# Performance work log

Hardware: AMD Instinct MI355X
Metric: run time of the kernel (lower is better)

Reference implementation:

```python
import jax, jax.numpy as jnp
import numpy as np

B, T, D, U = 32, 512, 512, 512  # batch, seq_len, input dim, lstm units


def setup_inputs() -> dict:
    key = jax.random.key(0)
    ks = jax.random.split(key, 8)
    s_in = 1.0 / np.sqrt(D)
    s_rec = 1.0 / np.sqrt(U)
    return {
        "x": jax.random.normal(ks[0], (B, T, D), dtype=jnp.float32),
        "z": jax.random.normal(ks[1], (B, U), dtype=jnp.float32) * 0.1,
        # forward-direction LSTM params (Keras gate order: i, f, c, o)
        "Wf": jax.random.normal(ks[2], (D, 4 * U), dtype=jnp.float32) * s_in,
        "Uf": jax.random.normal(ks[3], (U, 4 * U), dtype=jnp.float32) * s_rec,
        "bf": jnp.zeros((4 * U,), dtype=jnp.float32),
        # backward-direction LSTM params
        "Wb": jax.random.normal(ks[4], (D, 4 * U), dtype=jnp.float32) * s_in,
        "Ub": jax.random.normal(ks[5], (U, 4 * U), dtype=jnp.float32) * s_rec,
        "bb": jnp.zeros((4 * U,), dtype=jnp.float32),
    }


def _lstm(x, h0, c0, W, Uw, b, reverse):
    """Single-direction LSTM, return_sequences=True. Keras gate order i,f,c,o."""
    u = h0.shape[-1]
    # precompute input projections for all timesteps in one big GEMM
    xg = jnp.einsum("btd,dk->btk", x, W) + b  # [B,T,4U]

    def step(carry, xg_t):
        h, c = carry
        g = xg_t + h @ Uw  # [B,4U]
        i = jax.nn.sigmoid(g[:, :u])
        f = jax.nn.sigmoid(g[:, u:2 * u])
        cc = jnp.tanh(g[:, 2 * u:3 * u])
        o = jax.nn.sigmoid(g[:, 3 * u:])
        c = f * c + i * cc
        h = o * jnp.tanh(c)
        return (h, c), h

    # scan over time; reverse=True == Keras go_backwards + output re-reversal
    _, hs = jax.lax.scan(step, (h0, c0), jnp.swapaxes(xg, 0, 1), reverse=reverse)
    return jnp.swapaxes(hs, 0, 1)  # [B,T,U]


def reference(x, z, Wf, Uf, bf, Wb, Ub, bb):
    # conditional=True: initial_state = [z, z, z, z] -> both directions get (h0=z, c0=z)
    fwd = _lstm(x, z, z, Wf, Uf, bf, reverse=False)
    bwd = _lstm(x, z, z, Wb, Ub, bb, reverse=True)
    return fwd + bwd  # Bidirectional merge_mode='sum', return_sequences=True
```

## Files before the change

kernel.cpp:

```cpp
#include <hip/hip_runtime.h>
#include <hip/hip_bf16.h>


typedef __attribute__((ext_vector_type(8))) __bf16 bf16x8;
typedef __attribute__((ext_vector_type(4))) __bf16 bf16x4;
typedef __attribute__((ext_vector_type(4))) float fvec4;

#define AS_G(p) ((const __attribute__((address_space(1))) void*)(p))
#define AS_L(p) ((__attribute__((address_space(3))) void*)(p))

__device__ __forceinline__ float sigm(float x) {
  return __builtin_amdgcn_rcpf(1.f + __expf(-x));
}
__device__ __forceinline__ float tanh_f(float x) {
  return 1.f - 2.f * __builtin_amdgcn_rcpf(__expf(2.f * x) + 1.f);
}

__device__ __forceinline__ void st_h4(__bf16* p, float h0, float h1) {
  union { __bf16 h[2]; unsigned int u; } pk;
  pk.h[0] = (__bf16)h0;
  pk.h[1] = (__bf16)h1;
  __hip_atomic_store((unsigned int*)p, pk.u, __ATOMIC_RELAXED, __HIP_MEMORY_SCOPE_AGENT);
}


__global__ void k_convert_x(const float* __restrict__ x, __bf16* __restrict__ xb) {
  size_t i = ((size_t)blockIdx.x * 256 + threadIdx.x) * 8;
  fvec4 a = *(const fvec4*)(x + i);
  fvec4 b = *(const fvec4*)(x + i + 4);
  bf16x8 o;
#pragma unroll
  for (int j = 0; j < 4; ++j) { o[j] = (__bf16)a[j]; o[4 + j] = (__bf16)b[j]; }
  *(bf16x8*)(xb + i) = o;
}

__global__ void k_build_T(const float* __restrict__ src, const float* __restrict__ bvec,
                          __bf16* __restrict__ dst, float* __restrict__ bias_out) {
  int p = blockIdx.x;
  int g = p >> 6, r = p & 63, w = r >> 4, q = r & 15, jj = q >> 2, gate = q & 3;
  int orig = gate * 512 + g * 16 + w * 4 + jj;
  for (int k = threadIdx.x; k < 512; k += 256)
    dst[(size_t)p * 512 + k] = (__bf16)src[(size_t)k * 2048 + orig];
  if (bias_out && threadIdx.x == 0) bias_out[p] = bvec[orig];
}

__global__ void k_init_flags(int* flags) {
  int i = blockIdx.x * 256 + threadIdx.x;
  if (i < 1024) flags[i] = 0;
}

__global__ void k_init_h(const float* __restrict__ z, __bf16* __restrict__ hbuf) {
  int idx = blockIdx.x * 256 + threadIdx.x;
  int dir = idx >> 14, rem = idx & 16383;
  int ks = rem >> 10, row = (rem >> 5) & 31, c = rem & 31;
  hbuf[(size_t)dir * 32768 + rem] = (__bf16)z[row * 512 + ks * 32 + c];
}


__global__ __launch_bounds__(256, 2) void k_gemm_xw(
    const __bf16* __restrict__ A,
    const __bf16* __restrict__ Bt,
    const float* __restrict__ bias,
    __bf16* __restrict__ C)
{
  __shared__ __align__(16) __bf16 As[128 * 32];
  __shared__ __align__(16) __bf16 Bs[128 * 32];
  const int tid = threadIdx.x;
  const int w = tid >> 6, lane = tid & 63, quad = lane >> 4, l15 = lane & 15;
  const int m0 = blockIdx.y * 128, n0 = blockIdx.x * 128;
  const int wm = w & 1, wn = w >> 1;

  fvec4 acc[4][4];
  const fvec4 zero = {0.f, 0.f, 0.f, 0.f};
#pragma unroll
  for (int i = 0; i < 4; ++i)
#pragma unroll
    for (int j = 0; j < 4; ++j) acc[i][j] = zero;

  for (int kb = 0; kb < 16; ++kb) {
    const int k0 = kb * 32;
#pragma unroll
    for (int i = 0; i < 2; ++i) {
      const int c = (i * 4 + w) * 64 + lane;
      const int row = c >> 2, kk = (c & 3) * 8;
      __builtin_amdgcn_global_load_lds(AS_G(A + (size_t)(m0 + row) * 512 + k0 + kk),
                                       AS_L(As + (size_t)(i * 4 + w) * 512), 16, 0, 0);
      __builtin_amdgcn_global_load_lds(AS_G(Bt + (size_t)(n0 + row) * 512 + k0 + kk),
                                       AS_L(Bs + (size_t)(i * 4 + w) * 512), 16, 0, 0);
    }
    __syncthreads();
    bf16x8 af[4], bfr[4];
#pragma unroll
    for (int mt = 0; mt < 4; ++mt)
      af[mt] = *(const bf16x8*)(As + (wm * 64 + mt * 16 + l15) * 32 + quad * 8);
#pragma unroll
    for (int nt = 0; nt < 4; ++nt)
      bfr[nt] = *(const bf16x8*)(Bs + (wn * 64 + nt * 16 + l15) * 32 + quad * 8);
#pragma unroll
    for (int mt = 0; mt < 4; ++mt)
#pragma unroll
      for (int nt = 0; nt < 4; ++nt)
        acc[mt][nt] = __builtin_amdgcn_mfma_f32_16x16x32_bf16(af[mt], bfr[nt], acc[mt][nt], 0, 0, 0);
    __syncthreads();
  }

#pragma unroll
  for (int nt = 0; nt < 4; ++nt) {
    const int col = n0 + wn * 64 + nt * 16 + l15;
    const float bv = bias[col];
#pragma unroll
    for (int mt = 0; mt < 4; ++mt) {
      const int rowb = m0 + wm * 64 + mt * 16 + quad * 4;
#pragma unroll
      for (int r = 0; r < 4; ++r)
        C[(size_t)(rowb + r) * 4096 + col] = (__bf16)(acc[mt][nt][r] + bv);
    }
  }
}


__global__ __launch_bounds__(256, 1) void k_lstm_rec(
    const __bf16* __restrict__ xg,
    const float* __restrict__ z,
    const __bf16* __restrict__ UT,
    __bf16* __restrict__ hbuf,
    float* __restrict__ outf,
    __bf16* __restrict__ outb,
    int* __restrict__ flags)
{
  const int blk = blockIdx.x, dir = blk >> 5, g = blk & 31;
  const int tid = threadIdx.x, w = tid >> 6, lane = tid & 63;
  const int quad = lane >> 4, l15 = lane & 15;
  __shared__ __align__(16) __bf16 h_lds[16384];
  __shared__ __align__(16) float gates[32][68];

  bf16x8 breg[16];
  {
    const __bf16* up = UT + ((size_t)dir * 2048 + g * 64 + w * 16 + l15) * 512 + quad * 8;
#pragma unroll
    for (int ks = 0; ks < 16; ++ks) breg[ks] = *(const bf16x8*)(up + ks * 32);
  }

  const int b = lane >> 1, jpair = lane & 1;
  const int hcol = g * 16 + w * 4 + jpair * 2;
  float c0 = z[b * 512 + hcol];
  float c1 = z[b * 512 + hcol + 1];
  int* myflags = flags + dir * 512;
  const __bf16* hsrc = hbuf + (size_t)dir * 32768;
  const int stoff = (g >> 1) * 1024 + b * 32 + (g & 1) * 16 + w * 4 + jpair * 2;
  const int stage_off = w * 4096 + lane * 8;
  const fvec4 zero = {0.f, 0.f, 0.f, 0.f};

  for (int kt = 0; kt < 512; ++kt) {
    const int t = dir ? (511 - kt) : kt;
    const int pr = kt & 1;

    const bf16x8 xv = *(const bf16x8*)(xg + (size_t)(b * 512 + t) * 4096 +
                                       dir * 2048 + g * 64 + w * 16 + jpair * 8);

    if (kt > 0) {
      const int* fl = myflags + (kt - 1);
      while (__hip_atomic_load(fl, __ATOMIC_RELAXED, __HIP_MEMORY_SCOPE_AGENT) < 32)
        __builtin_amdgcn_s_sleep(1);
    }

    {
      const unsigned long long* src =
          (const unsigned long long*)(hsrc + pr * 16384 + stage_off);
      unsigned long long tmp[16];
#pragma unroll
      for (int it = 0; it < 8; ++it) {
        tmp[2 * it]     = __hip_atomic_load(src + it * 128,
                            __ATOMIC_RELAXED, __HIP_MEMORY_SCOPE_AGENT);
        tmp[2 * it + 1] = __hip_atomic_load(src + it * 128 + 1,
                            __ATOMIC_RELAXED, __HIP_MEMORY_SCOPE_AGENT);
      }
      __bf16* dst = h_lds + stage_off;
#pragma unroll
      for (int it = 0; it < 8; ++it) {
        union { unsigned long long u[2]; bf16x8 v; } cv;
        cv.u[0] = tmp[2 * it];
        cv.u[1] = tmp[2 * it + 1];
        *(bf16x8*)(dst + it * 512) = cv.v;
      }
    }
    __syncthreads();

    fvec4 acc0 = zero, acc1 = zero;
#pragma unroll 8
    for (int ks = 0; ks < 16; ++ks) {
      bf16x8 a0 = *(const bf16x8*)(h_lds + ks * 1024 + l15 * 32 + quad * 8);
      bf16x8 a1 = *(const bf16x8*)(h_lds + ks * 1024 + (16 + l15) * 32 + quad * 8);
      acc0 = __builtin_amdgcn_mfma_f32_16x16x32_bf16(a0, breg[ks], acc0, 0, 0, 0);
      acc1 = __builtin_amdgcn_mfma_f32_16x16x32_bf16(a1, breg[ks], acc1, 0, 0, 0);
    }

#pragma unroll
    for (int r = 0; r < 4; ++r) {
      gates[quad * 4 + r][w * 16 + l15] = acc0[r];
      gates[16 + quad * 4 + r][w * 16 + l15] = acc1[r];
    }
    const fvec4 gA = *(const fvec4*)&gates[b][w * 16 + jpair * 8];
    const fvec4 gB = *(const fvec4*)&gates[b][w * 16 + jpair * 8 + 4];

    float xf[8];
#pragma unroll
    for (int j = 0; j < 8; ++j) xf[j] = (float)xv[j];

    float ii = sigm(gA[0] + xf[0]);
    float ff = sigm(gA[1] + xf[1]);
    float cc = tanh_f(gA[2] + xf[2]);
    float oo = sigm(gA[3] + xf[3]);
    c0 = ff * c0 + ii * cc;
    const float h0 = oo * tanh_f(c0);

    ii = sigm(gB[0] + xf[4]);
    ff = sigm(gB[1] + xf[5]);
    cc = tanh_f(gB[2] + xf[6]);
    oo = sigm(gB[3] + xf[7]);
    c1 = ff * c1 + ii * cc;
    const float h1 = oo * tanh_f(c1);

    st_h4(hbuf + (size_t)dir * 32768 + ((kt + 1) & 1) * 16384 + stoff, h0, h1);

    __syncthreads();
    if (tid == 0)
      __hip_atomic_fetch_add(myflags + kt, 1, __ATOMIC_RELAXED, __HIP_MEMORY_SCOPE_AGENT);

    const size_t oidx = (size_t)(b * 512 + t) * 512 + hcol;
    if (dir == 0) {
      outf[oidx] = h0;
      outf[oidx + 1] = h1;
    } else {
      outb[oidx] = (__bf16)h0;
      outb[oidx + 1] = (__bf16)h1;
    }
  }
}


__global__ void k_add_bwd(float* __restrict__ out, const __bf16* __restrict__ outb) {
  size_t i = ((size_t)blockIdx.x * 256 + threadIdx.x) * 4;
  if (i >= (size_t)32 * 512 * 512) return;
  fvec4 o = *(const fvec4*)(out + i);
  bf16x4 bv = *(const bf16x4*)(outb + i);
#pragma unroll
  for (int j = 0; j < 4; ++j) o[j] += (float)bv[j];
  *(fvec4*)(out + i) = o;
}


extern "C" void kernel_launch(void* const* d_in, const int* in_sizes, int n_in,
                              void* d_out, int out_size, void* d_ws, size_t ws_size,
                              hipStream_t stream) {
  const float* x  = (const float*)d_in[0];
  const float* z  = (const float*)d_in[1];
  const float* Wf = (const float*)d_in[2];
  const float* Uf = (const float*)d_in[3];
  const float* bf = (const float*)d_in[4];
  const float* Wb = (const float*)d_in[5];
  const float* Ub = (const float*)d_in[6];
  const float* bb = (const float*)d_in[7];
  float* out = (float*)d_out;
  char* ws = (char*)d_ws;

  size_t off = 0;
  __bf16* xg    = (__bf16*)(ws + off); off += (size_t)16384 * 4096 * 2;
  __bf16* UT    = (__bf16*)(ws + off); off += (size_t)2 * 2048 * 512 * 2;
  __bf16* hbuf  = (__bf16*)(ws + off); off += (size_t)2 * 2 * 16384 * 2;
  int*    flags = (int*)(ws + off);    off += 4096;
  float*  biasp = (float*)(ws + off);  off += 4096 * 4;
  char* uni = ws + off;
  __bf16* xb   = (__bf16*)uni;
  __bf16* WT   = (__bf16*)(uni + (size_t)16384 * 512 * 2);
  __bf16* outb = (__bf16*)uni;

  k_convert_x<<<4096, 256, 0, stream>>>(x, xb);
  k_build_T<<<2048, 256, 0, stream>>>(Wf, bf, WT, biasp);
  k_build_T<<<2048, 256, 0, stream>>>(Wb, bb, WT + (size_t)2048 * 512, biasp + 2048);
  k_build_T<<<2048, 256, 0, stream>>>(Uf, nullptr, UT, nullptr);
  k_build_T<<<2048, 256, 0, stream>>>(Ub, nullptr, UT + (size_t)2048 * 512, nullptr);
  k_init_flags<<<4, 256, 0, stream>>>(flags);
  k_init_h<<<128, 256, 0, stream>>>(z, hbuf);
  k_gemm_xw<<<dim3(32, 128), 256, 0, stream>>>(xb, WT, biasp, xg);
  k_lstm_rec<<<64, 256, 0, stream>>>(xg, z, UT, hbuf, out, outb, flags);
  k_add_bwd<<<8192, 256, 0, stream>>>(out, outb);
}
```

Before: 2.266 ms.

## Replace atomic step counter with per-block mailbox flags and swizzle LDS h tile

Cross-block step synchronization changes from one shared atomic counter per timestep to a mailbox matrix. Each block stores its completed step into a private slot, and wave 0 polls all producers' slots in parallel with a ballot before a block barrier. This removes contention from 32 blocks atomically incrementing the same word each step. The staged hidden-state tile in LDS is also XOR-swizzled so the MFMA A-fragment reads hit fewer bank conflicts. The trade-off is an extra barrier per step and more polling traffic.

Result: faster. 2.205 ms (-2.7%).

```diff
diff --git a/kernel.cpp b/kernel.cpp
--- a/kernel.cpp
+++ b/kernel.cpp
@@ -44,9 +44,9 @@
   if (bias_out && threadIdx.x == 0) bias_out[p] = bvec[orig];
 }
 
-__global__ void k_init_flags(int* flags) {
+__global__ void k_init_flags(int* mbox) {
   int i = blockIdx.x * 256 + threadIdx.x;
-  if (i < 1024) flags[i] = 0;
+  if (i < 2048) mbox[i] = 0;
 }
 
 __global__ void k_init_h(const float* __restrict__ z, __bf16* __restrict__ hbuf) {
@@ -126,7 +126,7 @@
     __bf16* __restrict__ hbuf,
     float* __restrict__ outf,
     __bf16* __restrict__ outb,
-    int* __restrict__ flags)
+    int* __restrict__ mbox)
 {
   const int blk = blockIdx.x, dir = blk >> 5, g = blk & 31;
   const int tid = threadIdx.x, w = tid >> 6, lane = tid & 63;
@@ -145,10 +145,13 @@
   const int hcol = g * 16 + w * 4 + jpair * 2;
   float c0 = z[b * 512 + hcol];
   float c1 = z[b * 512 + hcol + 1];
-  int* myflags = flags + dir * 512;
   const __bf16* hsrc = hbuf + (size_t)dir * 32768;
   const int stoff = (g >> 1) * 1024 + b * 32 + (g & 1) * 16 + w * 4 + jpair * 2;
   const int stage_off = w * 4096 + lane * 8;
+  const int swz8 = ((lane & 3) ^ ((lane >> 3) & 3)) * 8;
+  const int fr_swz = ((l15 >> 1) & 3);
+  int* my_line = mbox + dir * 1024 + g * 32;
+  int* my_col  = mbox + dir * 1024 + lane * 32 + g;
   const fvec4 zero = {0.f, 0.f, 0.f, 0.f};
 
   for (int kt = 0; kt < 512; ++kt) {
@@ -159,9 +162,15 @@
                                        dir * 2048 + g * 64 + w * 16 + jpair * 8);
 
     if (kt > 0) {
-      const int* fl = myflags + (kt - 1);
-      while (__hip_atomic_load(fl, __ATOMIC_RELAXED, __HIP_MEMORY_SCOPE_AGENT) < 32)
-        __builtin_amdgcn_s_sleep(1);
+      if (w == 0) {
+        const int* mb = my_line + (lane & 31);
+        for (;;) {
+          int v = __hip_atomic_load(mb, __ATOMIC_RELAXED, __HIP_MEMORY_SCOPE_AGENT);
+          if (!__ballot(lane < 32 && v < kt)) break;
+          __builtin_amdgcn_s_sleep(1);
+        }
+      }
+      __syncthreads();
     }
 
     {
@@ -175,13 +184,13 @@
         tmp[2 * it + 1] = __hip_atomic_load(src + it * 128 + 1,
                             __ATOMIC_RELAXED, __HIP_MEMORY_SCOPE_AGENT);
       }
-      __bf16* dst = h_lds + stage_off;
 #pragma unroll
       for (int it = 0; it < 8; ++it) {
         union { unsigned long long u[2]; bf16x8 v; } cv;
         cv.u[0] = tmp[2 * it];
         cv.u[1] = tmp[2 * it + 1];
-        *(bf16x8*)(dst + it * 512) = cv.v;
+        *(bf16x8*)(h_lds + (w * 4 + (it >> 1)) * 1024 +
+                   ((it & 1) * 16 + (lane >> 2)) * 32 + swz8) = cv.v;
       }
     }
     __syncthreads();
@@ -189,8 +198,10 @@
     fvec4 acc0 = zero, acc1 = zero;
 #pragma unroll 8
     for (int ks = 0; ks < 16; ++ks) {
-      bf16x8 a0 = *(const bf16x8*)(h_lds + ks * 1024 + l15 * 32 + quad * 8);
-      bf16x8 a1 = *(const bf16x8*)(h_lds + ks * 1024 + (16 + l15) * 32 + quad * 8);
+      bf16x8 a0 = *(const bf16x8*)(h_lds + ks * 1024 + l15 * 32 +
+                                   ((quad ^ fr_swz) * 8));
+      bf16x8 a1 = *(const bf16x8*)(h_lds + ks * 1024 + (16 + l15) * 32 +
+                                   ((quad ^ fr_swz) * 8));
       acc0 = __builtin_amdgcn_mfma_f32_16x16x32_bf16(a0, breg[ks], acc0, 0, 0, 0);
       acc1 = __builtin_amdgcn_mfma_f32_16x16x32_bf16(a1, breg[ks], acc1, 0, 0, 0);
     }
@@ -224,8 +235,8 @@
     st_h4(hbuf + (size_t)dir * 32768 + ((kt + 1) & 1) * 16384 + stoff, h0, h1);
 
     __syncthreads();
-    if (tid == 0)
-      __hip_atomic_fetch_add(myflags + kt, 1, __ATOMIC_RELAXED, __HIP_MEMORY_SCOPE_AGENT);
+    if (w == 0 && lane < 32)
+      __hip_atomic_store(my_col, kt + 1, __ATOMIC_RELAXED, __HIP_MEMORY_SCOPE_AGENT);
 
     const size_t oidx = (size_t)(b * 512 + t) * 512 + hcol;
     if (dir == 0) {
@@ -268,7 +279,7 @@
   __bf16* xg    = (__bf16*)(ws + off); off += (size_t)16384 * 4096 * 2;
   __bf16* UT    = (__bf16*)(ws + off); off += (size_t)2 * 2048 * 512 * 2;
   __bf16* hbuf  = (__bf16*)(ws + off); off += (size_t)2 * 2 * 16384 * 2;
-  int*    flags = (int*)(ws + off);    off += 4096;
+  int*    mbox  = (int*)(ws + off);    off += 8192;
   float*  biasp = (float*)(ws + off);  off += 4096 * 4;
   char* uni = ws + off;
   __bf16* xb   = (__bf16*)uni;
@@ -280,9 +291,9 @@
   k_build_T<<<2048, 256, 0, stream>>>(Wb, bb, WT + (size_t)2048 * 512, biasp + 2048);
   k_build_T<<<2048, 256, 0, stream>>>(Uf, nullptr, UT, nullptr);
   k_build_T<<<2048, 256, 0, stream>>>(Ub, nullptr, UT + (size_t)2048 * 512, nullptr);
-  k_init_flags<<<4, 256, 0, stream>>>(flags);
+  k_init_flags<<<8, 256, 0, stream>>>(mbox);
   k_init_h<<<128, 256, 0, stream>>>(z, hbuf);
   k_gemm_xw<<<dim3(32, 128), 256, 0, stream>>>(xb, WT, biasp, xg);
-  k_lstm_rec<<<64, 256, 0, stream>>>(xg, z, UT, hbuf, out, outb, flags);
+  k_lstm_rec<<<64, 256, 0, stream>>>(xg, z, UT, hbuf, out, outb, mbox);
   k_add_bwd<<<8192, 256, 0, stream>>>(out, outb);
 }
```
